# Performance work log

Hardware: AMD Instinct MI355X
Metric: run time of the kernel (lower is better)

## Reference

```python
import jax, jax.numpy as jnp
import numpy as np

B, N, CIN = 4, 8192, 256
H, D = 8, 64            # n_heads, head_n_channels
INNER = H * D           # 512
COUT = 256
EPS = 1e-5              # torch InstanceNorm1d default eps


def setup_inputs() -> dict:
    key = jax.random.key(0)
    ks = jax.random.split(key, 8)
    s = 1.0 / np.sqrt(CIN)
    return {
        "u_x": jax.random.normal(ks[0], (B, N, CIN), dtype=jnp.float32),
        "pos_x": jax.random.uniform(ks[1], (B, N, 2), dtype=jnp.float32),
        # torch nn.Linear weights have shape (out_features, in_features)
        "Wq": jax.random.normal(ks[2], (INNER, CIN), dtype=jnp.float32) * s,
        "Wk": jax.random.normal(ks[3], (INNER, CIN), dtype=jnp.float32) * s,
        "Wv": jax.random.normal(ks[4], (INNER, CIN), dtype=jnp.float32) * s,
        "Wo": jax.random.normal(ks[5], (COUT, INNER), dtype=jnp.float32) * (1.0 / np.sqrt(INNER)),
        "bo": jax.random.normal(ks[6], (COUT,), dtype=jnp.float32) * 0.01,
    }


def _heads(x, W):
    # x: [B,N,CIN] @ W.T -> [B,N,H*D] -> [B,H,N,D]
    y = jnp.einsum("bnc,ec->bne", x, W)
    return y.reshape(x.shape[0], x.shape[1], H, D).transpose(0, 2, 1, 3)


def _inorm(u):
    # Matches torch: InstanceNorm1d applied to (B*H, N, D) normalizes over the
    # LAST dim (D) per (batch, head, grid point), biased variance, no affine.
    mean = jnp.mean(u, axis=-1, keepdims=True)
    var = jnp.mean(jnp.square(u - mean), axis=-1, keepdims=True)
    return (u - mean) / jnp.sqrt(var + EPS)


def reference(u_x, pos_x, Wq, Wk, Wv, Wo, bo):
    batch, n = u_x.shape[0], u_x.shape[1]
    q = _heads(u_x, Wq)          # [B,H,N,D]
    k = _inorm(_heads(u_x, Wk))  # u_y = u_x (self-attention path)
    v = _inorm(_heads(u_x, Wv))
    # associative path: (K^T V) then Q; uniform weights = 1/N
    dots = jnp.einsum("bhnd,bhne->bhde", k, v)   # [B,H,D,D]
    u = jnp.einsum("bhnd,bhde->bhne", q, dots) / n
    u = u.transpose(0, 2, 1, 3).reshape(batch, n, INNER)
    return jnp.einsum("bne,oe->bno", u, Wo) + bo
```

## Files before the change

kernel.cpp:

```cpp
#include <hip/hip_runtime.h>


#define B_    4
#define N_    8192
#define CIN_  256
#define H_    8
#define D_    64
#define INNER_ 512
#define COUT_ 256
#define EPS_  1e-5f

typedef unsigned short ushort_t;
typedef unsigned int   uint_t;
typedef __attribute__((ext_vector_type(8))) short short8;
typedef __attribute__((ext_vector_type(4))) float f32x4;

__device__ __forceinline__ void split_bf16(float x, ushort_t& hi, ushort_t& lo) {
  const uint_t u = __float_as_uint(x);
  const uint_t hr = (u + 0x8000u) & 0xffff0000u;
  hi = (ushort_t)(hr >> 16);
  const float l = x - __uint_as_float(hr);
  lo = (ushort_t)((__float_as_uint(l) + 0x8000u) >> 16);
}

__device__ __forceinline__ void cvt8(float4 x, float4 y, uint4& uh, uint4& ul) {
  const float v[8] = {x.x, x.y, x.z, x.w, y.x, y.y, y.z, y.w};
  ushort_t h[8], l[8];
#pragma unroll
  for (int j = 0; j < 8; j++) split_bf16(v[j], h[j], l[j]);
  uh = make_uint4(h[0] | ((uint_t)h[1] << 16), h[2] | ((uint_t)h[3] << 16),
                  h[4] | ((uint_t)h[5] << 16), h[6] | ((uint_t)h[7] << 16));
  ul = make_uint4(l[0] | ((uint_t)l[1] << 16), l[2] | ((uint_t)l[3] << 16),
                  l[4] | ((uint_t)l[5] << 16), l[6] | ((uint_t)l[7] << 16));
}

#define MFMA(A, Bv, C) __builtin_amdgcn_mfma_f32_16x16x32_bf16((A), (Bv), (C), 0, 0, 0)

__global__ __launch_bounds__(256) void prep_all_kernel(
    const float* __restrict__ u_x, const float* __restrict__ Wk,
    const float* __restrict__ Wv, ushort_t* __restrict__ uxH,
    ushort_t* __restrict__ uxL, ushort_t* __restrict__ WkvH,
    ushort_t* __restrict__ WkvL, float* __restrict__ dots)
{
  const int bid = blockIdx.x;
  if (bid < 4096) {
    const size_t base = ((size_t)bid * 256 + threadIdx.x) * 8;
    const float4 x = *(const float4*)(u_x + base);
    const float4 y = *(const float4*)(u_x + base + 4);
    uint4 uh, ul;
    cvt8(x, y, uh, ul);
    *(uint4*)(uxH + base) = uh;
    *(uint4*)(uxL + base) = ul;
  } else {
    const int wb = bid - 4096;
    const size_t base = ((size_t)wb * 256 + threadIdx.x) * 8;
    const float* src = (base < 131072) ? (Wk + base) : (Wv + base - 131072);
    const float4 x = *(const float4*)(src);
    const float4 y = *(const float4*)(src + 4);
    uint4 uh, ul;
    cvt8(x, y, uh, ul);
    *(uint4*)(WkvH + base) = uh;
    *(uint4*)(WkvL + base) = ul;
    *(float4*)(dots + ((size_t)wb * 256 + threadIdx.x) * 4) =
        make_float4(0.f, 0.f, 0.f, 0.f);
  }
}

__global__ __launch_bounds__(256, 2) void kv_dots_kernel(
    const ushort_t* __restrict__ uxH, const ushort_t* __restrict__ uxL,
    const ushort_t* __restrict__ WkvH, const ushort_t* __restrict__ WkvL,
    float* __restrict__ dots)
{
  __shared__ __align__(16) char smem[69632];
  ushort_t* KtH = (ushort_t*)(smem);
  ushort_t* KtL = (ushort_t*)(smem + 17408);
  ushort_t* VtH = (ushort_t*)(smem + 34816);
  ushort_t* VtL = (ushort_t*)(smem + 52224);

  const int t = threadIdx.x;
  const int chunk = blockIdx.x, h = blockIdx.y, b = blockIdx.z;
  const int lane = t & 63, wave = t >> 6;
  const int q = lane >> 4, r = lane & 15;
  const int m0 = (wave >> 1) * 64, n0 = (wave & 1) * 64;
  const int srow = t >> 1, scs = (t & 1) * 16, q0 = (t & 1) * 2;
  const int dstripe = 16 * wave;

  const int wr = (srow < 64) ? (h * 64 + srow) : (512 + h * 64 + srow - 64);
  const ushort_t* bgH = WkvH + (size_t)wr * CIN_ + scs;
  const ushort_t* bgL = WkvL + (size_t)wr * CIN_ + scs;

  f32x4 dacc[4];
#pragma unroll
  for (int j = 0; j < 4; j++) dacc[j] = (f32x4)0.f;

  for (int mt = 0; mt < 2; mt++) {
    const int r0 = chunk * 256 + mt * 128;
    const ushort_t* agH = uxH + ((size_t)(b * N_) + r0 + srow) * CIN_ + scs;
    const ushort_t* agL = uxL + ((size_t)(b * N_) + r0 + srow) * CIN_ + scs;

    f32x4 acc[4][4];
#pragma unroll
    for (int i = 0; i < 4; i++)
#pragma unroll
      for (int j = 0; j < 4; j++) acc[i][j] = (f32x4)0.f;

    {
      const uint4 a0 = *(const uint4*)(agH);
      const uint4 a1 = *(const uint4*)(agH + 8);
      const uint4 l0 = *(const uint4*)(agL);
      const uint4 l1 = *(const uint4*)(agL + 8);
      const uint4 b0 = *(const uint4*)(bgH);
      const uint4 b1 = *(const uint4*)(bgH + 8);
      const uint4 c0 = *(const uint4*)(bgL);
      const uint4 c1 = *(const uint4*)(bgL + 8);
      ushort_t (*Ah)[130][8] = (ushort_t(*)[130][8])(smem);
      ushort_t (*Al)[130][8] = (ushort_t(*)[130][8])(smem + 8320);
      ushort_t (*Bh)[130][8] = (ushort_t(*)[130][8])(smem + 16640);
      ushort_t (*Bl)[130][8] = (ushort_t(*)[130][8])(smem + 24960);
      *(uint4*)&Ah[q0][srow][0] = a0;  *(uint4*)&Ah[q0 + 1][srow][0] = a1;
      *(uint4*)&Al[q0][srow][0] = l0;  *(uint4*)&Al[q0 + 1][srow][0] = l1;
      *(uint4*)&Bh[q0][srow][0] = b0;  *(uint4*)&Bh[q0 + 1][srow][0] = b1;
      *(uint4*)&Bl[q0][srow][0] = c0;  *(uint4*)&Bl[q0 + 1][srow][0] = c1;
    }
    __syncthreads();

#pragma unroll 2
    for (int kc = 0; kc < 8; kc++) {
      const int cur = kc & 1, nxt = cur ^ 1;
      uint4 a0, a1, l0, l1, b0, b1, c0, c1;
      if (kc < 7) {
        const int off = (kc + 1) * 32;
        a0 = *(const uint4*)(agH + off);  a1 = *(const uint4*)(agH + off + 8);
        l0 = *(const uint4*)(agL + off);  l1 = *(const uint4*)(agL + off + 8);
        b0 = *(const uint4*)(bgH + off);  b1 = *(const uint4*)(bgH + off + 8);
        c0 = *(const uint4*)(bgL + off);  c1 = *(const uint4*)(bgL + off + 8);
      }
      char* sc = smem + cur * 33280;
      ushort_t (*Ah)[130][8] = (ushort_t(*)[130][8])(sc);
      ushort_t (*Al)[130][8] = (ushort_t(*)[130][8])(sc + 8320);
      ushort_t (*Bh)[130][8] = (ushort_t(*)[130][8])(sc + 16640);
      ushort_t (*Bl)[130][8] = (ushort_t(*)[130][8])(sc + 24960);
      short8 ahf[4], alf[4];
#pragma unroll
      for (int mi = 0; mi < 4; mi++) {
        ahf[mi] = *(const short8*)&Ah[q][m0 + 16 * mi + r][0];
        alf[mi] = *(const short8*)&Al[q][m0 + 16 * mi + r][0];
      }
#pragma unroll
      for (int nj = 0; nj < 4; nj++) {
        const short8 bhv = *(const short8*)&Bh[q][n0 + 16 * nj + r][0];
        const short8 blv = *(const short8*)&Bl[q][n0 + 16 * nj + r][0];
#pragma unroll
        for (int mi = 0; mi < 4; mi++) {
          acc[mi][nj] = MFMA(ahf[mi], bhv, acc[mi][nj]);
          acc[mi][nj] = MFMA(alf[mi], bhv, acc[mi][nj]);
          acc[mi][nj] = MFMA(ahf[mi], blv, acc[mi][nj]);
        }
      }
      if (kc < 7) {
        char* sn = smem + nxt * 33280;
        ushort_t (*nAh)[130][8] = (ushort_t(*)[130][8])(sn);
        ushort_t (*nAl)[130][8] = (ushort_t(*)[130][8])(sn + 8320);
        ushort_t (*nBh)[130][8] = (ushort_t(*)[130][8])(sn + 16640);
        ushort_t (*nBl)[130][8] = (ushort_t(*)[130][8])(sn + 24960);
        *(uint4*)&nAh[q0][srow][0] = a0;  *(uint4*)&nAh[q0 + 1][srow][0] = a1;
        *(uint4*)&nAl[q0][srow][0] = l0;  *(uint4*)&nAl[q0 + 1][srow][0] = l1;
        *(uint4*)&nBh[q0][srow][0] = b0;  *(uint4*)&nBh[q0 + 1][srow][0] = b1;
        *(uint4*)&nBl[q0][srow][0] = c0;  *(uint4*)&nBl[q0 + 1][srow][0] = c1;
      }
      __syncthreads();
    }

    float mean[4][4], inv[4][4];
#pragma unroll
    for (int mi = 0; mi < 4; mi++)
#pragma unroll
      for (int reg = 0; reg < 4; reg++) {
        float rs = 0.f, rq = 0.f;
#pragma unroll
        for (int nj = 0; nj < 4; nj++) {
          const float v = acc[mi][nj][reg];
          rs += v;
          rq = fmaf(v, v, rq);
        }
#pragma unroll
        for (int msk = 1; msk < 16; msk <<= 1) {
          rs += __shfl_xor(rs, msk, 64);
          rq += __shfl_xor(rq, msk, 64);
        }
        const float m = rs * (1.f / 64.f);
        const float var = fmaxf(rq * (1.f / 64.f) - m * m, 0.f);
        mean[mi][reg] = m;
        inv[mi][reg] = rsqrtf(var + EPS_);
      }

    {
      ushort_t* DH = (wave & 1) ? VtH : KtH;
      ushort_t* DL = (wave & 1) ? VtL : KtL;
#pragma unroll
      for (int nj = 0; nj < 4; nj++) {
        const int d = 16 * nj + r;
#pragma unroll
        for (int mi = 0; mi < 4; mi++) {
          const int cc = m0 + 16 * mi + 4 * q;
          ushort_t hh[4], ll[4];
#pragma unroll
          for (int reg = 0; reg < 4; reg++) {
            const float v = (acc[mi][nj][reg] - mean[mi][reg]) * inv[mi][reg];
            split_bf16(v, hh[reg], ll[reg]);
          }
          uint2 ph, pl;
          ph.x = hh[0] | ((uint_t)hh[1] << 16);
          ph.y = hh[2] | ((uint_t)hh[3] << 16);
          pl.x = ll[0] | ((uint_t)ll[1] << 16);
          pl.y = ll[2] | ((uint_t)ll[3] << 16);
          *(uint2*)&DH[d * 136 + cc] = ph;
          *(uint2*)&DL[d * 136 + cc] = pl;
        }
      }
    }
    __syncthreads();

#pragma unroll
    for (int ks = 0; ks < 4; ks++) {
      const short8 aH = *(const short8*)&KtH[(dstripe + r) * 136 + ks * 32 + q * 8];
      const short8 aL = *(const short8*)&KtL[(dstripe + r) * 136 + ks * 32 + q * 8];
#pragma unroll
      for (int ej = 0; ej < 4; ej++) {
        const short8 bH = *(const short8*)&VtH[(16 * ej + r) * 136 + ks * 32 + q * 8];
        const short8 bL = *(const short8*)&VtL[(16 * ej + r) * 136 + ks * 32 + q * 8];
        dacc[ej] = MFMA(aH, bH, dacc[ej]);
        dacc[ej] = MFMA(aL, bH, dacc[ej]);
        dacc[ej] = MFMA(aH, bL, dacc[ej]);
      }
    }
    __syncthreads();
  }

  float* dg = dots + ((size_t)(b * H_ + h)) * 4096;
#pragma unroll
  for (int ej = 0; ej < 4; ej++)
#pragma unroll
    for (int reg = 0; reg < 4; reg++)
      atomicAdd(&dg[(dstripe + 4 * q + reg) * 64 + 16 * ej + r], dacc[ej][reg]);
}

__global__ __launch_bounds__(256) void mid_kernel(
    const float* __restrict__ dots, const float* __restrict__ Wo,
    const float* __restrict__ Wq, ushort_t* __restrict__ MbtH,
    ushort_t* __restrict__ MbtL)
{
  __shared__ float WoL[8][520];
  __shared__ float S_loc[512][9];
  const int o0 = blockIdx.x * 8, b = blockIdx.y;
  const int t = threadIdx.x;

#pragma unroll
  for (int i = 0; i < 16; i++) {
    const int idx = i * 256 + t;
    WoL[idx >> 9][idx & 511] = Wo[(size_t)(o0 + (idx >> 9)) * INNER_ + (idx & 511)];
  }
  __syncthreads();

#pragma unroll
  for (int hh = 0; hh < 2; hh++) {
    const int hd = hh * 256 + t, h = hd >> 6, d = hd & 63;
    const float* dr = dots + ((size_t)(b * H_ + h)) * 4096 + d * 64;
    float row[64];
#pragma unroll
    for (int e = 0; e < 64; e += 4) *(float4*)&row[e] = *(const float4*)(dr + e);
#pragma unroll
    for (int o = 0; o < 8; o++) {
      float s = 0.f;
#pragma unroll
      for (int e = 0; e < 64; e++) s = fmaf(row[e], WoL[o][h * 64 + e], s);
      S_loc[hd][o] = s;
    }
  }
  __syncthreads();

  float acc[8];
#pragma unroll
  for (int o = 0; o < 8; o++) acc[o] = 0.f;
#pragma unroll 8
  for (int hd = 0; hd < INNER_; hd++) {
    const float w = Wq[(size_t)hd * CIN_ + t];
#pragma unroll
    for (int o = 0; o < 8; o++) acc[o] = fmaf(w, S_loc[hd][o], acc[o]);
  }
#pragma unroll
  for (int o = 0; o < 8; o++) {
    const float v = acc[o] * (1.0f / N_);
    ushort_t hi, lo;
    split_bf16(v, hi, lo);
    const size_t off = ((size_t)(b * COUT_) + o0 + o) * CIN_ + t;
    MbtH[off] = hi;
    MbtL[off] = lo;
  }
}

__global__ __launch_bounds__(256, 4) void out_kernel(
    const ushort_t* __restrict__ uxH, const ushort_t* __restrict__ uxL,
    const ushort_t* __restrict__ MbtH, const ushort_t* __restrict__ MbtL,
    const float* __restrict__ bo, float* __restrict__ out)
{
  __shared__ __align__(16) char smem[33280];
  ushort_t (*Ah)[130][8] = (ushort_t(*)[130][8])(smem);
  ushort_t (*Al)[130][8] = (ushort_t(*)[130][8])(smem + 8320);
  ushort_t (*Bh)[130][8] = (ushort_t(*)[130][8])(smem + 16640);
  ushort_t (*Bl)[130][8] = (ushort_t(*)[130][8])(smem + 24960);

  const int t = threadIdx.x;
  const int r0 = blockIdx.x * 128, o0 = blockIdx.y * 128, b = blockIdx.z;
  const int lane = t & 63, wave = t >> 6;
  const int q = lane >> 4, r = lane & 15;
  const int m0 = (wave >> 1) * 64, n0 = (wave & 1) * 64;
  const int srow = t >> 1, scs = (t & 1) * 16, q0 = (t & 1) * 2;

  const ushort_t* agH = uxH + ((size_t)(b * N_) + r0 + srow) * CIN_ + scs;
  const ushort_t* agL = uxL + ((size_t)(b * N_) + r0 + srow) * CIN_ + scs;
  const ushort_t* bgH = MbtH + ((size_t)(b * COUT_) + o0 + srow) * CIN_ + scs;
  const ushort_t* bgL = MbtL + ((size_t)(b * COUT_) + o0 + srow) * CIN_ + scs;

  f32x4 acc[4][4];
#pragma unroll
  for (int i = 0; i < 4; i++)
#pragma unroll
    for (int j = 0; j < 4; j++) acc[i][j] = (f32x4)0.f;

  for (int kc = 0; kc < 8; kc++) {
    *(uint4*)&Ah[q0][srow][0]     = *(const uint4*)(agH + kc * 32);
    *(uint4*)&Ah[q0 + 1][srow][0] = *(const uint4*)(agH + kc * 32 + 8);
    *(uint4*)&Al[q0][srow][0]     = *(const uint4*)(agL + kc * 32);
    *(uint4*)&Al[q0 + 1][srow][0] = *(const uint4*)(agL + kc * 32 + 8);
    *(uint4*)&Bh[q0][srow][0]     = *(const uint4*)(bgH + kc * 32);
    *(uint4*)&Bh[q0 + 1][srow][0] = *(const uint4*)(bgH + kc * 32 + 8);
    *(uint4*)&Bl[q0][srow][0]     = *(const uint4*)(bgL + kc * 32);
    *(uint4*)&Bl[q0 + 1][srow][0] = *(const uint4*)(bgL + kc * 32 + 8);
    __syncthreads();
    short8 ahf[4], alf[4];
#pragma unroll
    for (int mi = 0; mi < 4; mi++) {
      ahf[mi] = *(const short8*)&Ah[q][m0 + 16 * mi + r][0];
      alf[mi] = *(const short8*)&Al[q][m0 + 16 * mi + r][0];
    }
#pragma unroll
    for (int nj = 0; nj < 4; nj++) {
      const short8 bhv = *(const short8*)&Bh[q][n0 + 16 * nj + r][0];
      const short8 blv = *(const short8*)&Bl[q][n0 + 16 * nj + r][0];
#pragma unroll
      for (int mi = 0; mi < 4; mi++) {
        acc[mi][nj] = MFMA(ahf[mi], bhv, acc[mi][nj]);
        acc[mi][nj] = MFMA(alf[mi], bhv, acc[mi][nj]);
        acc[mi][nj] = MFMA(ahf[mi], blv, acc[mi][nj]);
      }
    }
    __syncthreads();
  }

  float bov[4];
#pragma unroll
  for (int nj = 0; nj < 4; nj++) bov[nj] = bo[o0 + n0 + 16 * nj + r];
#pragma unroll
  for (int mi = 0; mi < 4; mi++)
#pragma unroll
    for (int nj = 0; nj < 4; nj++) {
      const f32x4 v = acc[mi][nj];
#pragma unroll
      for (int reg = 0; reg < 4; reg++) {
        const int row = r0 + m0 + 16 * mi + q * 4 + reg;
        out[((size_t)(b * N_) + row) * COUT_ + o0 + n0 + 16 * nj + r] =
            v[reg] + bov[nj];
      }
    }
}

extern "C" void kernel_launch(void* const* d_in, const int* in_sizes, int n_in,
                              void* d_out, int out_size, void* d_ws, size_t ws_size,
                              hipStream_t stream) {
  const float* u_x = (const float*)d_in[0];
  const float* Wq = (const float*)d_in[2];
  const float* Wk = (const float*)d_in[3];
  const float* Wv = (const float*)d_in[4];
  const float* Wo = (const float*)d_in[5];
  const float* bo = (const float*)d_in[6];
  float* out = (float*)d_out;

  ushort_t* uxH  = (ushort_t*)d_ws;
  ushort_t* uxL  = uxH + 8388608;
  ushort_t* WkvH = uxL + 8388608;
  ushort_t* WkvL = WkvH + 262144;
  ushort_t* MbtH = WkvL + 262144;
  ushort_t* MbtL = MbtH + 262144;
  float* dots = (float*)(MbtL + 262144);

  prep_all_kernel<<<4224, 256, 0, stream>>>(u_x, Wk, Wv, uxH, uxL, WkvH, WkvL, dots);
  kv_dots_kernel<<<dim3(32, 8, 4), 256, 0, stream>>>(uxH, uxL, WkvH, WkvL, dots);
  mid_kernel<<<dim3(32, 4), 256, 0, stream>>>(dots, Wo, Wq, MbtH, MbtL);
  out_kernel<<<dim3(64, 2, 4), 256, 0, stream>>>(uxH, uxL, MbtH, MbtL, bo, out);
}
```

Before: 231.1 us.

## Load GEMM tiles with direct global-to-LDS DMA and shrink kv_dots LDS footprint

Replaces register-staged global loads and LDS stores in kv_dots and out kernels with global_load_lds 16-byte direct copies into unpadded tiles. kv_dots drops its software double buffer and splits the per-tile normalize-and-dot stage into two half passes, so it can use a smaller K/V transpose buffer and run at higher occupancy (launch bounds 4). The aim is to cut VGPR pressure and load/store instruction overhead. The cost is losing explicit prefetch overlap, possible LDS bank conflicts from the removed padding, and extra barriers.

```diff
diff --git a/kernel.cpp b/kernel.cpp
--- a/kernel.cpp
+++ b/kernel.cpp
@@ -35,6 +35,12 @@
 }
 
 #define MFMA(A, Bv, C) __builtin_amdgcn_mfma_f32_16x16x32_bf16((A), (Bv), (C), 0, 0, 0)
+
+__device__ __forceinline__ void dma16(const ushort_t* gsrc, void* ldsbase) {
+  __builtin_amdgcn_global_load_lds(
+      (const __attribute__((address_space(1))) unsigned int*)gsrc,
+      (__attribute__((address_space(3))) unsigned int*)ldsbase, 16, 0, 0);
+}
 
 __global__ __launch_bounds__(256) void prep_all_kernel(
     const float* __restrict__ u_x, const float* __restrict__ Wk,
@@ -66,28 +72,32 @@
   }
 }
 
-__global__ __launch_bounds__(256, 2) void kv_dots_kernel(
+__global__ __launch_bounds__(256, 4) void kv_dots_kernel(
     const ushort_t* __restrict__ uxH, const ushort_t* __restrict__ uxL,
     const ushort_t* __restrict__ WkvH, const ushort_t* __restrict__ WkvL,
     float* __restrict__ dots)
 {
-  __shared__ __align__(16) char smem[69632];
+  __shared__ __align__(16) char smem[36864];
+  ushort_t (*Ah)[128][8] = (ushort_t(*)[128][8])(smem);
+  ushort_t (*Al)[128][8] = (ushort_t(*)[128][8])(smem + 8192);
+  ushort_t (*Bh)[128][8] = (ushort_t(*)[128][8])(smem + 16384);
+  ushort_t (*Bl)[128][8] = (ushort_t(*)[128][8])(smem + 24576);
   ushort_t* KtH = (ushort_t*)(smem);
-  ushort_t* KtL = (ushort_t*)(smem + 17408);
-  ushort_t* VtH = (ushort_t*)(smem + 34816);
-  ushort_t* VtL = (ushort_t*)(smem + 52224);
+  ushort_t* KtL = (ushort_t*)(smem + 9216);
+  ushort_t* VtH = (ushort_t*)(smem + 18432);
+  ushort_t* VtL = (ushort_t*)(smem + 27648);
 
   const int t = threadIdx.x;
   const int chunk = blockIdx.x, h = blockIdx.y, b = blockIdx.z;
   const int lane = t & 63, wave = t >> 6;
   const int q = lane >> 4, r = lane & 15;
   const int m0 = (wave >> 1) * 64, n0 = (wave & 1) * 64;
-  const int srow = t >> 1, scs = (t & 1) * 16, q0 = (t & 1) * 2;
   const int dstripe = 16 * wave;
 
-  const int wr = (srow < 64) ? (h * 64 + srow) : (512 + h * 64 + srow - 64);
-  const ushort_t* bgH = WkvH + (size_t)wr * CIN_ + scs;
-  const ushort_t* bgL = WkvL + (size_t)wr * CIN_ + scs;
+  const ushort_t* bsrc0H = WkvH + (size_t)(h * 64 + lane) * CIN_ + wave * 8;
+  const ushort_t* bsrc0L = WkvL + (size_t)(h * 64 + lane) * CIN_ + wave * 8;
+  const ushort_t* bsrc1H = WkvH + (size_t)(512 + h * 64 + lane) * CIN_ + wave * 8;
+  const ushort_t* bsrc1L = WkvL + (size_t)(512 + h * 64 + lane) * CIN_ + wave * 8;
 
   f32x4 dacc[4];
 #pragma unroll
@@ -95,8 +105,11 @@
 
   for (int mt = 0; mt < 2; mt++) {
     const int r0 = chunk * 256 + mt * 128;
-    const ushort_t* agH = uxH + ((size_t)(b * N_) + r0 + srow) * CIN_ + scs;
-    const ushort_t* agL = uxL + ((size_t)(b * N_) + r0 + srow) * CIN_ + scs;
+    const ushort_t* asrc0H = uxH + ((size_t)(b * N_) + r0 + lane) * CIN_ + wave * 8;
+    const ushort_t* asrc0L = uxL + ((size_t)(b * N_) + r0 + lane) * CIN_ + wave * 8;
+    const ushort_t* asrc1H = asrc0H + (size_t)64 * CIN_;
+    const ushort_t* asrc1L = asrc0L + (size_t)64 * CIN_;
+    char* const pa = smem + wave * 2048;
 
     f32x4 acc[4][4];
 #pragma unroll
@@ -104,42 +117,17 @@
 #pragma unroll
       for (int j = 0; j < 4; j++) acc[i][j] = (f32x4)0.f;
 
-    {
-      const uint4 a0 = *(const uint4*)(agH);
-      const uint4 a1 = *(const uint4*)(agH + 8);
-      const uint4 l0 = *(const uint4*)(agL);
-      const uint4 l1 = *(const uint4*)(agL + 8);
-      const uint4 b0 = *(const uint4*)(bgH);
-      const uint4 b1 = *(const uint4*)(bgH + 8);
-      const uint4 c0 = *(const uint4*)(bgL);
-      const uint4 c1 = *(const uint4*)(bgL + 8);
-      ushort_t (*Ah)[130][8] = (ushort_t(*)[130][8])(smem);
-      ushort_t (*Al)[130][8] = (ushort_t(*)[130][8])(smem + 8320);
-      ushort_t (*Bh)[130][8] = (ushort_t(*)[130][8])(smem + 16640);
-      ushort_t (*Bl)[130][8] = (ushort_t(*)[130][8])(smem + 24960);
-      *(uint4*)&Ah[q0][srow][0] = a0;  *(uint4*)&Ah[q0 + 1][srow][0] = a1;
-      *(uint4*)&Al[q0][srow][0] = l0;  *(uint4*)&Al[q0 + 1][srow][0] = l1;
-      *(uint4*)&Bh[q0][srow][0] = b0;  *(uint4*)&Bh[q0 + 1][srow][0] = b1;
-      *(uint4*)&Bl[q0][srow][0] = c0;  *(uint4*)&Bl[q0 + 1][srow][0] = c1;
-    }
-    __syncthreads();
-
-#pragma unroll 2
     for (int kc = 0; kc < 8; kc++) {
-      const int cur = kc & 1, nxt = cur ^ 1;
-      uint4 a0, a1, l0, l1, b0, b1, c0, c1;
-      if (kc < 7) {
-        const int off = (kc + 1) * 32;
-        a0 = *(const uint4*)(agH + off);  a1 = *(const uint4*)(agH + off + 8);
-        l0 = *(const uint4*)(agL + off);  l1 = *(const uint4*)(agL + off + 8);
-        b0 = *(const uint4*)(bgH + off);  b1 = *(const uint4*)(bgH + off + 8);
-        c0 = *(const uint4*)(bgL + off);  c1 = *(const uint4*)(bgL + off + 8);
-      }
-      char* sc = smem + cur * 33280;
-      ushort_t (*Ah)[130][8] = (ushort_t(*)[130][8])(sc);
-      ushort_t (*Al)[130][8] = (ushort_t(*)[130][8])(sc + 8320);
-      ushort_t (*Bh)[130][8] = (ushort_t(*)[130][8])(sc + 16640);
-      ushort_t (*Bl)[130][8] = (ushort_t(*)[130][8])(sc + 24960);
+      const int ko = kc * 32;
+      dma16(asrc0H + ko, pa);
+      dma16(asrc1H + ko, pa + 1024);
+      dma16(asrc0L + ko, pa + 8192);
+      dma16(asrc1L + ko, pa + 9216);
+      dma16(bsrc0H + ko, pa + 16384);
+      dma16(bsrc1H + ko, pa + 17408);
+      dma16(bsrc0L + ko, pa + 24576);
+      dma16(bsrc1L + ko, pa + 25600);
+      __syncthreads();
       short8 ahf[4], alf[4];
 #pragma unroll
       for (int mi = 0; mi < 4; mi++) {
@@ -157,84 +145,71 @@
           acc[mi][nj] = MFMA(ahf[mi], blv, acc[mi][nj]);
         }
       }
-      if (kc < 7) {
-        char* sn = smem + nxt * 33280;
-        ushort_t (*nAh)[130][8] = (ushort_t(*)[130][8])(sn);
-        ushort_t (*nAl)[130][8] = (ushort_t(*)[130][8])(sn + 8320);
-        ushort_t (*nBh)[130][8] = (ushort_t(*)[130][8])(sn + 16640);
-        ushort_t (*nBl)[130][8] = (ushort_t(*)[130][8])(sn + 24960);
-        *(uint4*)&nAh[q0][srow][0] = a0;  *(uint4*)&nAh[q0 + 1][srow][0] = a1;
-        *(uint4*)&nAl[q0][srow][0] = l0;  *(uint4*)&nAl[q0 + 1][srow][0] = l1;
-        *(uint4*)&nBh[q0][srow][0] = b0;  *(uint4*)&nBh[q0 + 1][srow][0] = b1;
-        *(uint4*)&nBl[q0][srow][0] = c0;  *(uint4*)&nBl[q0 + 1][srow][0] = c1;
-      }
       __syncthreads();
     }
 
-    float mean[4][4], inv[4][4];
-#pragma unroll
-    for (int mi = 0; mi < 4; mi++)
-#pragma unroll
-      for (int reg = 0; reg < 4; reg++) {
-        float rs = 0.f, rq = 0.f;
-#pragma unroll
-        for (int nj = 0; nj < 4; nj++) {
-          const float v = acc[mi][nj][reg];
-          rs += v;
-          rq = fmaf(v, v, rq);
+    for (int p = 0; p < 2; p++) {
+      if ((wave >> 1) == p) {
+        ushort_t* DH = (wave & 1) ? VtH : KtH;
+        ushort_t* DL = (wave & 1) ? VtL : KtL;
+#pragma unroll
+        for (int mi = 0; mi < 4; mi++) {
+          float mean[4], inv[4];
+#pragma unroll
+          for (int reg = 0; reg < 4; reg++) {
+            float rs = 0.f, rq = 0.f;
+#pragma unroll
+            for (int nj = 0; nj < 4; nj++) {
+              const float v = acc[mi][nj][reg];
+              rs += v;
+              rq = fmaf(v, v, rq);
+            }
+#pragma unroll
+            for (int msk = 1; msk < 16; msk <<= 1) {
+              rs += __shfl_xor(rs, msk, 64);
+              rq += __shfl_xor(rq, msk, 64);
+            }
+            const float m = rs * (1.f / 64.f);
+            const float var = fmaxf(rq * (1.f / 64.f) - m * m, 0.f);
+            mean[reg] = m;
+            inv[reg] = rsqrtf(var + EPS_);
+          }
+          const int cc = 16 * mi + 4 * q;
+#pragma unroll
+          for (int nj = 0; nj < 4; nj++) {
+            const int d = 16 * nj + r;
+            ushort_t hh[4], ll[4];
+#pragma unroll
+            for (int reg = 0; reg < 4; reg++) {
+              const float v = (acc[mi][nj][reg] - mean[reg]) * inv[reg];
+              split_bf16(v, hh[reg], ll[reg]);
+            }
+            uint2 ph, pl;
+            ph.x = hh[0] | ((uint_t)hh[1] << 16);
+            ph.y = hh[2] | ((uint_t)hh[3] << 16);
+            pl.x = ll[0] | ((uint_t)ll[1] << 16);
+            pl.y = ll[2] | ((uint_t)ll[3] << 16);
+            *(uint2*)&DH[d * 72 + cc] = ph;
+            *(uint2*)&DL[d * 72 + cc] = pl;
+          }
         }
-#pragma unroll
-        for (int msk = 1; msk < 16; msk <<= 1) {
-          rs += __shfl_xor(rs, msk, 64);
-          rq += __shfl_xor(rq, msk, 64);
+      }
+      __syncthreads();
+#pragma unroll
+      for (int ks = 0; ks < 2; ks++) {
+        const short8 aH = *(const short8*)&KtH[(dstripe + r) * 72 + ks * 32 + q * 8];
+        const short8 aL = *(const short8*)&KtL[(dstripe + r) * 72 + ks * 32 + q * 8];
+#pragma unroll
+        for (int ej = 0; ej < 4; ej++) {
+          const short8 bH = *(const short8*)&VtH[(16 * ej + r) * 72 + ks * 32 + q * 8];
+          const short8 bL = *(const short8*)&VtL[(16 * ej + r) * 72 + ks * 32 + q * 8];
+          dacc[ej] = MFMA(aH, bH, dacc[ej]);
+          dacc[ej] = MFMA(aL, bH, dacc[ej]);
+          dacc[ej] = MFMA(aH, bL, dacc[ej]);
         }
-        const float m = rs * (1.f / 64.f);
-        const float var = fmaxf(rq * (1.f / 64.f) - m * m, 0.f);
-        mean[mi][reg] = m;
-        inv[mi][reg] = rsqrtf(var + EPS_);
-      }
-
-    {
-      ushort_t* DH = (wave & 1) ? VtH : KtH;
-      ushort_t* DL = (wave & 1) ? VtL : KtL;
-#pragma unroll
-      for (int nj = 0; nj < 4; nj++) {
-        const int d = 16 * nj + r;
-#pragma unroll
-        for (int mi = 0; mi < 4; mi++) {
-          const int cc = m0 + 16 * mi + 4 * q;
-          ushort_t hh[4], ll[4];
-#pragma unroll
-          for (int reg = 0; reg < 4; reg++) {
-            const float v = (acc[mi][nj][reg] - mean[mi][reg]) * inv[mi][reg];
-            split_bf16(v, hh[reg], ll[reg]);
-          }
-          uint2 ph, pl;
-          ph.x = hh[0] | ((uint_t)hh[1] << 16);
-          ph.y = hh[2] | ((uint_t)hh[3] << 16);
-          pl.x = ll[0] | ((uint_t)ll[1] << 16);
-          pl.y = ll[2] | ((uint_t)ll[3] << 16);
-          *(uint2*)&DH[d * 136 + cc] = ph;
-          *(uint2*)&DL[d * 136 + cc] = pl;
-        }
-      }
-    }
-    __syncthreads();
-
-#pragma unroll
-    for (int ks = 0; ks < 4; ks++) {
-      const short8 aH = *(const short8*)&KtH[(dstripe + r) * 136 + ks * 32 + q * 8];
-      const short8 aL = *(const short8*)&KtL[(dstripe + r) * 136 + ks * 32 + q * 8];
-#pragma unroll
-      for (int ej = 0; ej < 4; ej++) {
-        const short8 bH = *(const short8*)&VtH[(16 * ej + r) * 136 + ks * 32 + q * 8];
-        const short8 bL = *(const short8*)&VtL[(16 * ej + r) * 136 + ks * 32 + q * 8];
-        dacc[ej] = MFMA(aH, bH, dacc[ej]);
-        dacc[ej] = MFMA(aL, bH, dacc[ej]);
-        dacc[ej] = MFMA(aH, bL, dacc[ej]);
-      }
-    }
-    __syncthreads();
+      }
+      __syncthreads();
+    }
   }
 
   float* dg = dots + ((size_t)(b * H_ + h)) * 4096;
@@ -304,23 +279,27 @@
     const ushort_t* __restrict__ MbtH, const ushort_t* __restrict__ MbtL,
     const float* __restrict__ bo, float* __restrict__ out)
 {
-  __shared__ __align__(16) char smem[33280];
-  ushort_t (*Ah)[130][8] = (ushort_t(*)[130][8])(smem);
-  ushort_t (*Al)[130][8] = (ushort_t(*)[130][8])(smem + 8320);
-  ushort_t (*Bh)[130][8] = (ushort_t(*)[130][8])(smem + 16640);
-  ushort_t (*Bl)[130][8] = (ushort_t(*)[130][8])(smem + 24960);
+  __shared__ __align__(16) char smem[32768];
+  ushort_t (*Ah)[128][8] = (ushort_t(*)[128][8])(smem);
+  ushort_t (*Al)[128][8] = (ushort_t(*)[128][8])(smem + 8192);
+  ushort_t (*Bh)[128][8] = (ushort_t(*)[128][8])(smem + 16384);
+  ushort_t (*Bl)[128][8] = (ushort_t(*)[128][8])(smem + 24576);
 
   const int t = threadIdx.x;
   const int r0 = blockIdx.x * 128, o0 = blockIdx.y * 128, b = blockIdx.z;
   const int lane = t & 63, wave = t >> 6;
   const int q = lane >> 4, r = lane & 15;
   const int m0 = (wave >> 1) * 64, n0 = (wave & 1) * 64;
-  const int srow = t >> 1, scs = (t & 1) * 16, q0 = (t & 1) * 2;
-
-  const ushort_t* agH = uxH + ((size_t)(b * N_) + r0 + srow) * CIN_ + scs;
-  const ushort_t* agL = uxL + ((size_t)(b * N_) + r0 + srow) * CIN_ + scs;
-  const ushort_t* bgH = MbtH + ((size_t)(b * COUT_) + o0 + srow) * CIN_ + scs;
-  const ushort_t* bgL = MbtL + ((size_t)(b * COUT_) + o0 + srow) * CIN_ + scs;
+
+  const ushort_t* asrc0H = uxH + ((size_t)(b * N_) + r0 + lane) * CIN_ + wave * 8;
+  const ushort_t* asrc0L = uxL + ((size_t)(b * N_) + r0 + lane) * CIN_ + wave * 8;
+  const ushort_t* asrc1H = asrc0H + (size_t)64 * CIN_;
+  const ushort_t* asrc1L = asrc0L + (size_t)64 * CIN_;
+  const ushort_t* bsrc0H = MbtH + ((size_t)(b * COUT_) + o0 + lane) * CIN_ + wave * 8;
+  const ushort_t* bsrc0L = MbtL + ((size_t)(b * COUT_) + o0 + lane) * CIN_ + wave * 8;
+  const ushort_t* bsrc1H = bsrc0H + (size_t)64 * CIN_;
+  const ushort_t* bsrc1L = bsrc0L + (size_t)64 * CIN_;
+  char* const pa = smem + wave * 2048;
 
   f32x4 acc[4][4];
 #pragma unroll
@@ -329,14 +308,15 @@
     for (int j = 0; j < 4; j++) acc[i][j] = (f32x4)0.f;
 
   for (int kc = 0; kc < 8; kc++) {
-    *(uint4*)&Ah[q0][srow][0]     = *(const uint4*)(agH + kc * 32);
-    *(uint4*)&Ah[q0 + 1][srow][0] = *(const uint4*)(agH + kc * 32 + 8);
-    *(uint4*)&Al[q0][srow][0]     = *(const uint4*)(agL + kc * 32);
-    *(uint4*)&Al[q0 + 1][srow][0] = *(const uint4*)(agL + kc * 32 + 8);
-    *(uint4*)&Bh[q0][srow][0]     = *(const uint4*)(bgH + kc * 32);
-    *(uint4*)&Bh[q0 + 1][srow][0] = *(const uint4*)(bgH + kc * 32 + 8);
-    *(uint4*)&Bl[q0][srow][0]     = *(const uint4*)(bgL + kc * 32);
-    *(uint4*)&Bl[q0 + 1][srow][0] = *(const uint4*)(bgL + kc * 32 + 8);
+    const int ko = kc * 32;
+    dma16(asrc0H + ko, pa);
+    dma16(asrc1H + ko, pa + 1024);
+    dma16(asrc0L + ko, pa + 8192);
+    dma16(asrc1L + ko, pa + 9216);
+    dma16(bsrc0H + ko, pa + 16384);
+    dma16(bsrc1H + ko, pa + 17408);
+    dma16(bsrc0L + ko, pa + 24576);
+    dma16(bsrc1L + ko, pa + 25600);
     __syncthreads();
     short8 ahf[4], alf[4];
 #pragma unroll
```

New measurement: 336.5 us. 1.46x slower.
